# Performance work log

Measured on AMD Instinct MI355X. Metric: run time of the kernel, lower is better.

## Reference

```python
import jax, jax.numpy as jnp
import numpy as np
import math

D_MODEL, N_HEADS, D_HEAD = 768, 12, 64
INIT_RANGE = 0.02
ROPE_BASE = 10000.0


def _rope_cos_sin(seq_len, d_head, dtype=jnp.float32):
    # theta_j = base^(-2j/d), positions m -> angles [T, d/2]
    inv_freq = 1.0 / (ROPE_BASE ** (jnp.arange(0, d_head, 2, dtype=jnp.float32) / d_head))
    ang = jnp.arange(seq_len, dtype=jnp.float32)[:, None] * inv_freq[None, :]
    return jnp.cos(ang).astype(dtype), jnp.sin(ang).astype(dtype)


def _apply_rope(x, cos, sin):
    # x: [b, t, h, d]; rotate consecutive (even, odd) pairs as complex numbers
    xr, xi = x[..., 0::2], x[..., 1::2]
    c = cos[None, :, None, :]
    s = sin[None, :, None, :]
    out_r = xr * c - xi * s
    out_i = xr * s + xi * c
    return jnp.stack([out_r, out_i], axis=-1).reshape(x.shape)


def setup_inputs() -> dict:
    key = jax.random.key(0)
    ks = jax.random.split(key, 5)
    B, T = 2, 2048
    x = jax.random.normal(ks[0], (B, T, D_MODEL), dtype=jnp.float32)
    W_Q = INIT_RANGE * jax.random.normal(ks[1], (N_HEADS, D_MODEL, D_HEAD), dtype=jnp.float32)
    W_K = INIT_RANGE * jax.random.normal(ks[2], (N_HEADS, D_MODEL, D_HEAD), dtype=jnp.float32)
    W_V = INIT_RANGE * jax.random.normal(ks[3], (N_HEADS, D_MODEL, D_HEAD), dtype=jnp.float32)
    W_O = INIT_RANGE * jax.random.normal(ks[4], (N_HEADS, D_HEAD, D_MODEL), dtype=jnp.float32)
    b_Q = jnp.zeros((N_HEADS, D_HEAD), dtype=jnp.float32)
    b_K = jnp.zeros((N_HEADS, D_HEAD), dtype=jnp.float32)
    b_V = jnp.zeros((N_HEADS, D_HEAD), dtype=jnp.float32)
    b_O = jnp.zeros((D_MODEL,), dtype=jnp.float32)
    return {"normalized_resid_pre": x, "W_Q": W_Q, "b_Q": b_Q, "W_K": W_K, "b_K": b_K,
            "W_V": W_V, "b_V": b_V, "W_O": W_O, "b_O": b_O}


def reference(normalized_resid_pre, W_Q, b_Q, W_K, b_K, W_V, b_V, W_O, b_O):
    x = normalized_resid_pre
    B, T, _ = x.shape
    cos, sin = _rope_cos_sin(T, D_HEAD, x.dtype)
    Q = jnp.einsum('btc,hcd->bthd', x, W_Q) + b_Q
    K = jnp.einsum('btc,hcd->bthd', x, W_K) + b_K
    V = jnp.einsum('btc,hcd->bthd', x, W_V) + b_V
    Q = _apply_rope(Q, cos, sin)
    K = _apply_rope(K, cos, sin)
    scores = jnp.einsum('bqhd,bkhd->bhqk', Q, K) / math.sqrt(D_HEAD)
    # Faithful to source: tril zeros upper triangle, then all exact zeros -> -inf
    tril = jnp.tril(jnp.ones((T, T), dtype=bool))
    z = jnp.where(tril[None, None], scores, 0.0)
    z = jnp.where(z == 0.0, -jnp.inf, z)
    probs = jax.nn.softmax(z, axis=-1)
    o = jnp.einsum('bhqk,bkhd->bqhd', probs, V)
    return jnp.einsum('bqhd,hdm->bqm', o, W_O) + b_O
```

## Files before the change

kernel.cpp:

```cpp
#include <hip/hip_runtime.h>

typedef unsigned short u16;
typedef unsigned int u32;
typedef short bf16x8 __attribute__((ext_vector_type(8)));
typedef float f32x4 __attribute__((ext_vector_type(4)));
typedef float f32x16 __attribute__((ext_vector_type(16)));

#define MFMA(a, b, c) __builtin_amdgcn_mfma_f32_16x16x32_bf16(a, b, c, 0, 0, 0)
#define MFMA32(a, b, c) __builtin_amdgcn_mfma_f32_32x32x16_bf16(a, b, c, 0, 0, 0)

__device__ __forceinline__ u16 f2bf(float f) {
  unsigned int u = __float_as_uint(f);
  u = (u + 0x7FFFu + ((u >> 16) & 1u)) >> 16;
  return (u16)u;
}

#define GLOAD16(gp, lp)                                                        \
  __builtin_amdgcn_global_load_lds(                                            \
      (const __attribute__((address_space(1))) void*)(gp),                     \
      (__attribute__((address_space(3))) void*)(lp), 16, 0, 0)

__global__ __launch_bounds__(256) void prep_all(
    const float* __restrict__ x, const float* __restrict__ WQ,
    const float* __restrict__ WK, const float* __restrict__ WV,
    const float* __restrict__ WO, float* __restrict__ cost, float* __restrict__ sint,
    u16* __restrict__ xb, u16* __restrict__ Wt, u16* __restrict__ WoT) {
  __shared__ float tile[32][33];
  const int bid = blockIdx.x, tid = threadIdx.x;

  if (bid < 256) {
    int idx = bid * 256 + tid;
    int t = idx >> 5, i = idx & 31;
    float invf = expf(-(float)i * 0.28782313662425572f);
    float ang = (float)t * invf;
    cost[idx] = cosf(ang);
    sint[idx] = sinf(ang);
  } else if (bid < 3328) {
    int i = ((bid - 256) * 256 + tid) * 4;
    float4 v = *(const float4*)(x + i);
    ushort4 o = make_ushort4(f2bf(v.x), f2bf(v.y), f2bf(v.z), f2bf(v.w));
    *(ushort4*)(xb + i) = o;
  } else if (bid < 5056) {
    const int pbid = bid - 3328;
    const int z = pbid / 48, rem = pbid - z * 48;
    const int y = rem / 24, xk = rem - y * 24;
    const int qkv = z / 12, h = z - qkv * 12;
    const float* W = (qkv == 0 ? WQ : qkv == 1 ? WK : WV) + (size_t)h * 768 * 64;
    const int k0 = xk * 32, d0 = y * 32;
    const int tx = tid & 31, ty = tid >> 5;
#pragma unroll
    for (int it = 0; it < 4; it++)
      tile[ty + it * 8][tx] = W[(size_t)(k0 + ty + it * 8) * 64 + d0 + tx];
    __syncthreads();
    u16* out = Wt + (size_t)(qkv * 768 + h * 64 + d0) * 768 + k0;
#pragma unroll
    for (int it = 0; it < 4; it++)
      out[(size_t)(ty + it * 8) * 768 + tx] = f2bf(tile[tx][ty + it * 8]);
  } else {
    const int wbid = bid - 5056;
    const int a0 = (wbid % 24) * 32, m0 = (wbid / 24) * 32;
    const int tx = tid & 31, ty = tid >> 5;
#pragma unroll
    for (int it = 0; it < 4; it++)
      tile[ty + it * 8][tx] = WO[(size_t)(a0 + ty + it * 8) * 768 + m0 + tx];
    __syncthreads();
#pragma unroll
    for (int it = 0; it < 4; it++)
      WoT[(size_t)(m0 + ty + it * 8) * 768 + a0 + tx] = f2bf(tile[tx][ty + it * 8]);
  }
}

template <int MODE>
__global__ __launch_bounds__(256) void gemm_bt(
    const u16* __restrict__ A, const u16* __restrict__ Bt, int K, int LDA, int LDB,
    const float* __restrict__ bQ, const float* __restrict__ bK, const float* __restrict__ bV,
    const float* __restrict__ cost, const float* __restrict__ sint,
    u16* __restrict__ Qb, u16* __restrict__ Kb, u16* __restrict__ Vt,
    const float* __restrict__ bO, float* __restrict__ Out) {
  __shared__ u16 As[3][64 * 32];
  __shared__ u16 Bs[3][128 * 32];
  const int tid = threadIdx.x;
  const int w = tid >> 6, l = tid & 63;
  const int lr = l >> 4, lc = l & 15;
  const int wr = w >> 1, wc = w & 1;

  const int id = blockIdx.x;
  const int xcd = id & 7, idx = id >> 3;
  const int m0 = (xcd * 8 + (idx & 7)) * 64;
  const int n0 = (idx >> 3) * 128;

  f32x4 acc[2][4];
#pragma unroll
  for (int mi = 0; mi < 2; mi++)
#pragma unroll
    for (int ni = 0; ni < 4; ni++) acc[mi][ni] = (f32x4){0.f, 0.f, 0.f, 0.f};

  const int srow = w * 16 + (l >> 2);
  const int sg = (l & 3) ^ ((l >> 3) & 3);
  const u16* ga = A + (size_t)(m0 + srow) * LDA + sg * 8;
  const u16* gb = Bt + (size_t)(n0 + srow) * LDB + sg * 8;

#define GSTAGE(t, bi)                                                   \
  {                                                                     \
    const int kk = (t) * 32;                                            \
    GLOAD16(ga + kk, &As[bi][w * 512]);                                 \
    GLOAD16(gb + kk, &Bs[bi][w * 512]);                                 \
    GLOAD16(gb + kk + (size_t)64 * LDB, &Bs[bi][2048 + w * 512]);       \
  }

  const int n = K >> 5;
  GSTAGE(0, 0);
  if (n > 1) GSTAGE(1, 1);

  for (int kt = 0; kt < n; kt++) {
    if (kt + 1 < n) asm volatile("s_waitcnt vmcnt(3)" ::: "memory");
    else            asm volatile("s_waitcnt vmcnt(0)" ::: "memory");
    __builtin_amdgcn_s_barrier();
    __builtin_amdgcn_sched_barrier(0);
    if (kt + 2 < n) GSTAGE(kt + 2, (kt + 2) % 3);

    const char* as = (const char*)As[kt % 3];
    const char* bs = (const char*)Bs[kt % 3];
    bf16x8 af[2], bfr[4];
#pragma unroll
    for (int mi = 0; mi < 2; mi++) {
      const int row = wr * 32 + mi * 16 + lc;
      af[mi] = *(const bf16x8*)(as + row * 64 + ((lr ^ ((row >> 1) & 3)) << 4));
    }
#pragma unroll
    for (int ni = 0; ni < 4; ni++) {
      const int row = wc * 64 + ni * 16 + lc;
      bfr[ni] = *(const bf16x8*)(bs + row * 64 + ((lr ^ ((row >> 1) & 3)) << 4));
    }
    __builtin_amdgcn_s_setprio(1);
#pragma unroll
    for (int mi = 0; mi < 2; mi++)
#pragma unroll
      for (int ni = 0; ni < 4; ni++)
        acc[mi][ni] = MFMA(af[mi], bfr[ni], acc[mi][ni]);
    __builtin_amdgcn_s_setprio(0);
  }
#undef GSTAGE

#pragma unroll
  for (int mi = 0; mi < 2; mi++) {
#pragma unroll
    for (int ni = 0; ni < 4; ni++) {
      const int col = n0 + wc * 64 + ni * 16 + lc;
      const int rowb = m0 + wr * 32 + mi * 16 + lr * 4;
      if (MODE == 0) {
        const int qkv = col / 768;
        const int rem = col - qkv * 768;
        const int h = rem >> 6, d = rem & 63, fi = d >> 1;
        const float bb = (qkv == 0 ? bQ : qkv == 1 ? bK : bV)[rem];
#pragma unroll
        for (int r = 0; r < 4; r++) {
          const int grow = rowb + r;
          const int t = grow & 2047;
          float v = acc[mi][ni][r] + bb;
          float pv = __shfl_xor(v, 1);
          if (qkv < 2) {
            const float c = cost[t * 32 + fi], s = sint[t * 32 + fi];
            float o = (d & 1) ? (pv * s + v * c) : (v * c - pv * s);
            if (qkv == 0) o *= 0.125f;
            (qkv == 0 ? Qb : Kb)[(size_t)grow * 768 + rem] = f2bf(o);
          } else {
            const int bidx = grow >> 11;
            Vt[((size_t)(bidx * 12 + h) * 64 + d) * 2048 + t] = f2bf(v);
          }
        }
      } else {
        const float bb = bO[col];
#pragma unroll
        for (int r = 0; r < 4; r++) {
          const int grow = rowb + r;
          Out[(size_t)grow * 768 + col] = acc[mi][ni][r] + bb;
        }
      }
    }
  }
}

__global__ __launch_bounds__(256, 2) void attn_kernel(
    const u16* __restrict__ Qb, const u16* __restrict__ Kb,
    const u16* __restrict__ Vt, u16* __restrict__ Ob) {
  __shared__ char Kls[4][8192];
  __shared__ char Vls[4][8192];
  char* scratch = (char*)Kls;

  const int id = blockIdx.x + 16 * blockIdx.y;
  const int s_ = id >> 3;
  const int bh = (id & 7) + 8 * (s_ % 3);
  const int xq = s_ / 3;
  const int b = bh / 12, h = bh - b * 12;
  const int tid = threadIdx.x, w = tid >> 6, l = tid & 63;
  const int lq = l & 31, hi = l >> 5;
  const int qhalf = w & 1, grp = w >> 1;

  const u16* kbase = Kb + (size_t)(b * 2048) * 768 + h * 64;
  const u16* vbase = Vt + (size_t)(bh * 64) * 2048;

  const int r8 = l >> 3;
  const int scol8 = (l & 7) ^ r8;
  const u16* ksrc = kbase + (size_t)(w * 16 + r8) * 768 + scol8 * 8;
  const u16* vsrc = vbase + (size_t)(w * 16 + r8) * 2048 + scol8 * 8;

#define STAGE(t, bi)                                                        \
  {                                                                         \
    const size_t ko = (size_t)(t) * 64 * 768;                               \
    const int vo = (t) * 64;                                                \
    GLOAD16(ksrc + ko,            &Kls[bi][w * 2048]);                      \
    GLOAD16(ksrc + ko + 8 * 768,  &Kls[bi][w * 2048 + 1024]);               \
    GLOAD16(vsrc + vo,            &Vls[bi][w * 2048]);                      \
    GLOAD16(vsrc + vo + 8 * 2048, &Vls[bi][w * 2048 + 1024]);               \
  }

  const int fswz = (lq & 7) << 4;

#pragma unroll 1
  for (int half = 0; half < 2; half++) {
    const int qblk = half == 0 ? 31 - xq : xq;
    const int n = qblk + 1;
    const int nsup = (n + 1) >> 1;

    bf16x8 qf[4];
    {
      const u16* qp = Qb + ((size_t)(b * 2048 + qblk * 64 + qhalf * 32 + lq)) * 768 +
                      h * 64 + hi * 8;
#pragma unroll
      for (int c = 0; c < 4; c++) qf[c] = *(const bf16x8*)(qp + c * 16);
    }

    float m_run = -INFINITY, l_run = 0.f;
    f32x16 acc2[2];
    acc2[0] = (f32x16)0.0f;
    acc2[1] = (f32x16)0.0f;

    STAGE(0, 0);
    if (n > 1) STAGE(1, 1);

    for (int p = 0; p < nsup; p++) {
      const int t0 = 2 * p;
      asm volatile("s_waitcnt vmcnt(0)" ::: "memory");
      __builtin_amdgcn_s_barrier();
      __builtin_amdgcn_sched_barrier(0);
      if (t0 + 2 < n) STAGE(t0 + 2, (t0 + 2) & 3);
      if (t0 + 3 < n) STAGE(t0 + 3, (t0 + 3) & 3);

      const int tile = t0 + grp;
      if (tile < n) {
        const int cur = tile & 3;

        f32x16 s2[2];
        s2[0] = (f32x16)0.0f;
        s2[1] = (f32x16)0.0f;
        __builtin_amdgcn_s_setprio(1);
#pragma unroll
        for (int c = 0; c < 4; c++) {
          const int cb = (c * 32 + hi * 16) ^ fswz;
          bf16x8 kf0 = *(const bf16x8*)(&Kls[cur][lq * 128] + cb);
          bf16x8 kf1 = *(const bf16x8*)(&Kls[cur][(32 + lq) * 128] + cb);
          s2[0] = MFMA32(kf0, qf[c], s2[0]);
          s2[1] = MFMA32(kf1, qf[c], s2[1]);
        }
        __builtin_amdgcn_s_setprio(0);

        if (tile == qblk) {
          const int qrel = qhalf * 32 + lq;
#pragma unroll
          for (int kt2 = 0; kt2 < 2; kt2++)
#pragma unroll
            for (int r = 0; r < 16; r++) {
              const int ko = kt2 * 32 + (r & 3) + 8 * (r >> 2) + 4 * hi;
              if (ko > qrel) s2[kt2][r] = -INFINITY;
            }
        }

        float pm = s2[0][0];
#pragma unroll
        for (int r = 1; r < 16; r++) pm = fmaxf(pm, s2[0][r]);
#pragma unroll
        for (int r = 0; r < 16; r++) pm = fmaxf(pm, s2[1][r]);
        pm = fmaxf(pm, __shfl_xor(pm, 32));

        const float mn = fmaxf(m_run, pm);
        const float alpha = __expf(m_run - mn);
        m_run = mn;

        float rs = 0.f;
        u32 pk[2][8];
#pragma unroll
        for (int kt2 = 0; kt2 < 2; kt2++)
#pragma unroll
          for (int j = 0; j < 8; j++) {
            float p0 = __expf(s2[kt2][2 * j] - mn);
            float p1 = __expf(s2[kt2][2 * j + 1] - mn);
            rs += p0 + p1;
            asm("v_cvt_pk_bf16_f32 %0, %1, %2" : "=v"(pk[kt2][j]) : "v"(p0), "v"(p1));
          }
        l_run = l_run * alpha + rs;

        union { u32 u[4]; bf16x8 v; } pf[4];
#pragma unroll
        for (int kq = 0; kq < 4; kq++) {
          const int kt2 = kq >> 1, i0 = 4 * (kq & 1);
          u32 a0 = pk[kt2][i0], b0 = pk[kt2][i0 + 2];
          u32 a1 = pk[kt2][i0 + 1], b1 = pk[kt2][i0 + 3];
          asm("v_permlane32_swap_b32 %0, %1" : "+v"(a0), "+v"(b0));
          asm("v_permlane32_swap_b32 %0, %1" : "+v"(a1), "+v"(b1));
          pf[kq].u[0] = a0; pf[kq].u[1] = a1; pf[kq].u[2] = b0; pf[kq].u[3] = b1;
        }

#pragma unroll
        for (int dh = 0; dh < 2; dh++)
#pragma unroll
          for (int r = 0; r < 16; r++) acc2[dh][r] *= alpha;

        __builtin_amdgcn_s_setprio(1);
#pragma unroll
        for (int dh = 0; dh < 2; dh++) {
          const char* vr = &Vls[cur][(dh * 32 + lq) * 128];
#pragma unroll
          for (int kq = 0; kq < 4; kq++) {
            bf16x8 vf = *(const bf16x8*)(vr + ((kq * 32 + hi * 16) ^ fswz));
            acc2[dh] = MFMA32(vf, pf[kq].v, acc2[dh]);
          }
        }
        __builtin_amdgcn_s_setprio(0);
      }
    }

    asm volatile("s_waitcnt lgkmcnt(0)" ::: "memory");
    __builtin_amdgcn_s_barrier();
    if (grp == 1) {
      float* sc = (float*)scratch + ((size_t)(w - 2) * 64 + l) * 34;
#pragma unroll
      for (int dh = 0; dh < 2; dh++)
#pragma unroll
        for (int r = 0; r < 16; r++) sc[dh * 16 + r] = acc2[dh][r];
      sc[32] = m_run;
      sc[33] = l_run;
    }
    asm volatile("s_waitcnt lgkmcnt(0)" ::: "memory");
    __builtin_amdgcn_s_barrier();
    if (grp == 0) {
      const float* sc = (const float*)scratch + ((size_t)w * 64 + l) * 34;
      const float m1 = sc[32], l1 = sc[33];
      const float M = fmaxf(m_run, m1);
      const float a0 = __expf(m_run - M);
      const float a1 = __expf(m1 - M);
      const float lm = l_run * a0 + l1 * a1;
      const float lt = lm + __shfl_xor(lm, 32);
      const float inv = 1.0f / lt;
      u16* ob = Ob + ((size_t)(b * 2048 + qblk * 64 + qhalf * 32 + lq)) * 768 + h * 64;
#pragma unroll
      for (int dh = 0; dh < 2; dh++)
#pragma unroll
        for (int g = 0; g < 4; g++) {
          ushort4 o4;
          o4.x = f2bf((acc2[dh][4 * g + 0] * a0 + sc[dh * 16 + 4 * g + 0] * a1) * inv);
          o4.y = f2bf((acc2[dh][4 * g + 1] * a0 + sc[dh * 16 + 4 * g + 1] * a1) * inv);
          o4.z = f2bf((acc2[dh][4 * g + 2] * a0 + sc[dh * 16 + 4 * g + 2] * a1) * inv);
          o4.w = f2bf((acc2[dh][4 * g + 3] * a0 + sc[dh * 16 + 4 * g + 3] * a1) * inv);
          *(ushort4*)(ob + dh * 32 + 8 * g + 4 * hi) = o4;
        }
    }
    asm volatile("s_waitcnt lgkmcnt(0)" ::: "memory");
    __builtin_amdgcn_s_barrier();
  }
#undef STAGE
}


extern "C" void kernel_launch(void* const* d_in, const int* in_sizes, int n_in,
                              void* d_out, int out_size, void* d_ws, size_t ws_size,
                              hipStream_t stream) {
  const float* x  = (const float*)d_in[0];
  const float* WQ = (const float*)d_in[1];
  const float* bQ = (const float*)d_in[2];
  const float* WK = (const float*)d_in[3];
  const float* bK = (const float*)d_in[4];
  const float* WV = (const float*)d_in[5];
  const float* bV = (const float*)d_in[6];
  const float* WO = (const float*)d_in[7];
  const float* bO = (const float*)d_in[8];

  char* ws = (char*)d_ws;
  u16* Xb    = (u16*)(ws + 0);
  u16* Wqkv  = (u16*)(ws + 6291456);
  u16* WoT   = (u16*)(ws + 9830400);
  u16* Qb    = (u16*)(ws + 11010048);
  u16* Kb    = (u16*)(ws + 17301504);
  u16* Vt    = (u16*)(ws + 23592960);
  u16* Ob    = (u16*)(ws + 29884416);
  float* cost = (float*)(ws + 36175872);
  float* sint = (float*)(ws + 36438016);

  prep_all<<<5632, 256, 0, stream>>>(x, WQ, WK, WV, WO, cost, sint, Xb, Wqkv, WoT);

  gemm_bt<0><<<1152, 256, 0, stream>>>(Xb, Wqkv, 768, 768, 768,
                                       bQ, bK, bV, cost, sint,
                                       Qb, Kb, Vt, nullptr, nullptr);
  attn_kernel<<<dim3(16, 24), 256, 0, stream>>>(Qb, Kb, Vt, Ob);
  gemm_bt<1><<<384, 256, 0, stream>>>(Ob, WoT, 768, 768, 768,
                                      nullptr, nullptr, nullptr, nullptr, nullptr,
                                      nullptr, nullptr, nullptr, bO, (float*)d_out);
}
```

Measured before the change: 107.3 us.

## Enlarge QKV GEMM tile with register-direct A loads; defer softmax rescale

```diff
diff --git a/kernel.cpp b/kernel.cpp
--- a/kernel.cpp
+++ b/kernel.cpp
@@ -70,12 +70,114 @@
   }
 }
 
-template <int MODE>
-__global__ __launch_bounds__(256) void gemm_bt(
-    const u16* __restrict__ A, const u16* __restrict__ Bt, int K, int LDA, int LDB,
+__global__ __launch_bounds__(256) void gemm_qkv(
+    const u16* __restrict__ A, const u16* __restrict__ Bt,
     const float* __restrict__ bQ, const float* __restrict__ bK, const float* __restrict__ bV,
     const float* __restrict__ cost, const float* __restrict__ sint,
-    u16* __restrict__ Qb, u16* __restrict__ Kb, u16* __restrict__ Vt,
+    u16* __restrict__ Qb, u16* __restrict__ Kb, u16* __restrict__ Vt) {
+  __shared__ u16 Bs[3][128 * 32];
+  const int tid = threadIdx.x;
+  const int w = tid >> 6, l = tid & 63;
+  const int lr = l >> 4, lc = l & 15;
+  const int wr = w >> 1, wc = w & 1;
+
+  const int id = blockIdx.x;
+  const int xcd = id & 7, idx = id >> 3;
+  const int m0 = (xcd * 4 + (idx & 3)) * 128;
+  const int n0 = (idx >> 2) * 128;
+
+  f32x4 acc[4][4];
+#pragma unroll
+  for (int mi = 0; mi < 4; mi++)
+#pragma unroll
+    for (int ni = 0; ni < 4; ni++) acc[mi][ni] = (f32x4){0.f, 0.f, 0.f, 0.f};
+
+  const int srow = w * 16 + (l >> 2);
+  const int sg = (l & 3) ^ ((l >> 3) & 3);
+  const u16* gb = Bt + (size_t)(n0 + srow) * 768 + sg * 8;
+  const u16* gA = A + (size_t)(m0 + wr * 64 + lc) * 768 + lr * 8;
+
+#define BSTAGE(t, bi)                                                   \
+  {                                                                     \
+    const int kk = (t) * 32;                                            \
+    GLOAD16(gb + kk, &Bs[bi][w * 512]);                                 \
+    GLOAD16(gb + kk + (size_t)64 * 768, &Bs[bi][2048 + w * 512]);       \
+  }
+#define ALOAD(dst, t)                                                   \
+  {                                                                     \
+    _Pragma("unroll")                                                   \
+    for (int mi = 0; mi < 4; mi++)                                      \
+      dst[mi] = *(const bf16x8*)(gA + (size_t)(mi * 16) * 768 + (t) * 32); \
+  }
+#define KITER(kt, afc, afn)                                                    \
+  {                                                                            \
+    asm volatile("s_waitcnt vmcnt(0)" ::: "memory");                           \
+    __builtin_amdgcn_s_barrier();                                              \
+    __builtin_amdgcn_sched_barrier(0);                                         \
+    if ((kt) + 2 < 24) BSTAGE((kt) + 2, ((kt) + 2) % 3);                       \
+    if ((kt) + 1 < 24) ALOAD(afn, (kt) + 1);                                   \
+    const char* bs = (const char*)Bs[(kt) % 3];                                \
+    bf16x8 bfr[4];                                                             \
+    _Pragma("unroll")                                                          \
+    for (int ni = 0; ni < 4; ni++) {                                           \
+      const int row = wc * 64 + ni * 16 + lc;                                  \
+      bfr[ni] = *(const bf16x8*)(bs + row * 64 + ((lr ^ ((row >> 1) & 3)) << 4)); \
+    }                                                                          \
+    __builtin_amdgcn_s_setprio(1);                                             \
+    _Pragma("unroll")                                                          \
+    for (int mi = 0; mi < 4; mi++)                                             \
+      _Pragma("unroll")                                                        \
+      for (int ni = 0; ni < 4; ni++)                                           \
+        acc[mi][ni] = MFMA(afc[mi], bfr[ni], acc[mi][ni]);                     \
+    __builtin_amdgcn_s_setprio(0);                                             \
+  }
+
+  bf16x8 afA[4], afB[4];
+  BSTAGE(0, 0);
+  BSTAGE(1, 1);
+  ALOAD(afA, 0);
+
+#pragma unroll 1
+  for (int p = 0; p < 12; p++) {
+    KITER(2 * p, afA, afB);
+    KITER(2 * p + 1, afB, afA);
+  }
+#undef KITER
+#undef ALOAD
+#undef BSTAGE
+
+#pragma unroll
+  for (int mi = 0; mi < 4; mi++) {
+#pragma unroll
+    for (int ni = 0; ni < 4; ni++) {
+      const int col = n0 + wc * 64 + ni * 16 + lc;
+      const int rowb = m0 + wr * 64 + mi * 16 + lr * 4;
+      const int qkv = col / 768;
+      const int rem = col - qkv * 768;
+      const int h = rem >> 6, d = rem & 63, fi = d >> 1;
+      const float bb = (qkv == 0 ? bQ : qkv == 1 ? bK : bV)[rem];
+#pragma unroll
+      for (int r = 0; r < 4; r++) {
+        const int grow = rowb + r;
+        const int t = grow & 2047;
+        float v = acc[mi][ni][r] + bb;
+        float pv = __shfl_xor(v, 1);
+        if (qkv < 2) {
+          const float c = cost[t * 32 + fi], s = sint[t * 32 + fi];
+          float o = (d & 1) ? (pv * s + v * c) : (v * c - pv * s);
+          if (qkv == 0) o *= 0.125f;
+          (qkv == 0 ? Qb : Kb)[(size_t)grow * 768 + rem] = f2bf(o);
+        } else {
+          const int bidx = grow >> 11;
+          Vt[((size_t)(bidx * 12 + h) * 64 + d) * 2048 + t] = f2bf(v);
+        }
+      }
+    }
+  }
+}
+
+__global__ __launch_bounds__(256) void gemm_out(
+    const u16* __restrict__ A, const u16* __restrict__ Bt,
     const float* __restrict__ bO, float* __restrict__ Out) {
   __shared__ u16 As[3][64 * 32];
   __shared__ u16 Bs[3][128 * 32];
@@ -97,27 +199,27 @@
 
   const int srow = w * 16 + (l >> 2);
   const int sg = (l & 3) ^ ((l >> 3) & 3);
-  const u16* ga = A + (size_t)(m0 + srow) * LDA + sg * 8;
-  const u16* gb = Bt + (size_t)(n0 + srow) * LDB + sg * 8;
+  const u16* ga = A + (size_t)(m0 + srow) * 768 + sg * 8;
+  const u16* gb = Bt + (size_t)(n0 + srow) * 768 + sg * 8;
 
 #define GSTAGE(t, bi)                                                   \
   {                                                                     \
     const int kk = (t) * 32;                                            \
     GLOAD16(ga + kk, &As[bi][w * 512]);                                 \
     GLOAD16(gb + kk, &Bs[bi][w * 512]);                                 \
-    GLOAD16(gb + kk + (size_t)64 * LDB, &Bs[bi][2048 + w * 512]);       \
-  }
-
-  const int n = K >> 5;
+    GLOAD16(gb + kk + (size_t)64 * 768, &Bs[bi][2048 + w * 512]);       \
+  }
+
+  const int nt = 24;
   GSTAGE(0, 0);
-  if (n > 1) GSTAGE(1, 1);
-
-  for (int kt = 0; kt < n; kt++) {
-    if (kt + 1 < n) asm volatile("s_waitcnt vmcnt(3)" ::: "memory");
-    else            asm volatile("s_waitcnt vmcnt(0)" ::: "memory");
+  GSTAGE(1, 1);
+
+  for (int kt = 0; kt < nt; kt++) {
+    if (kt + 1 < nt) asm volatile("s_waitcnt vmcnt(3)" ::: "memory");
+    else             asm volatile("s_waitcnt vmcnt(0)" ::: "memory");
     __builtin_amdgcn_s_barrier();
     __builtin_amdgcn_sched_barrier(0);
-    if (kt + 2 < n) GSTAGE(kt + 2, (kt + 2) % 3);
+    if (kt + 2 < nt) GSTAGE(kt + 2, (kt + 2) % 3);
 
     const char* as = (const char*)As[kt % 3];
     const char* bs = (const char*)Bs[kt % 3];
@@ -148,34 +250,11 @@
     for (int ni = 0; ni < 4; ni++) {
       const int col = n0 + wc * 64 + ni * 16 + lc;
       const int rowb = m0 + wr * 32 + mi * 16 + lr * 4;
-      if (MODE == 0) {
-        const int qkv = col / 768;
-        const int rem = col - qkv * 768;
-        const int h = rem >> 6, d = rem & 63, fi = d >> 1;
-        const float bb = (qkv == 0 ? bQ : qkv == 1 ? bK : bV)[rem];
-#pragma unroll
-        for (int r = 0; r < 4; r++) {
-          const int grow = rowb + r;
-          const int t = grow & 2047;
-          float v = acc[mi][ni][r] + bb;
-          float pv = __shfl_xor(v, 1);
-          if (qkv < 2) {
-            const float c = cost[t * 32 + fi], s = sint[t * 32 + fi];
-            float o = (d & 1) ? (pv * s + v * c) : (v * c - pv * s);
-            if (qkv == 0) o *= 0.125f;
-            (qkv == 0 ? Qb : Kb)[(size_t)grow * 768 + rem] = f2bf(o);
-          } else {
-            const int bidx = grow >> 11;
-            Vt[((size_t)(bidx * 12 + h) * 64 + d) * 2048 + t] = f2bf(v);
-          }
-        }
-      } else {
-        const float bb = bO[col];
-#pragma unroll
-        for (int r = 0; r < 4; r++) {
-          const int grow = rowb + r;
-          Out[(size_t)grow * 768 + col] = acc[mi][ni][r] + bb;
-        }
+      const float bb = bO[col];
+#pragma unroll
+      for (int r = 0; r < 4; r++) {
+        const int grow = rowb + r;
+        Out[(size_t)grow * 768 + col] = acc[mi][ni][r] + bb;
       }
     }
   }
@@ -283,9 +362,17 @@
         for (int r = 0; r < 16; r++) pm = fmaxf(pm, s2[1][r]);
         pm = fmaxf(pm, __shfl_xor(pm, 32));
 
-        const float mn = fmaxf(m_run, pm);
-        const float alpha = __expf(m_run - mn);
-        m_run = mn;
+        const bool defer = __all(pm <= m_run + 8.0f);
+        if (!defer) {
+          const float mn = fmaxf(m_run, pm);
+          const float alpha = __expf(m_run - mn);
+          m_run = mn;
+          l_run *= alpha;
+#pragma unroll
+          for (int dh = 0; dh < 2; dh++)
+#pragma unroll
+            for (int r = 0; r < 16; r++) acc2[dh][r] *= alpha;
+        }
 
         float rs = 0.f;
         u32 pk[2][8];
@@ -293,12 +380,12 @@
         for (int kt2 = 0; kt2 < 2; kt2++)
 #pragma unroll
           for (int j = 0; j < 8; j++) {
-            float p0 = __expf(s2[kt2][2 * j] - mn);
-            float p1 = __expf(s2[kt2][2 * j + 1] - mn);
+            float p0 = __expf(s2[kt2][2 * j] - m_run);
+            float p1 = __expf(s2[kt2][2 * j + 1] - m_run);
             rs += p0 + p1;
             asm("v_cvt_pk_bf16_f32 %0, %1, %2" : "=v"(pk[kt2][j]) : "v"(p0), "v"(p1));
           }
-        l_run = l_run * alpha + rs;
+        l_run += rs;
 
         union { u32 u[4]; bf16x8 v; } pf[4];
 #pragma unroll
@@ -310,11 +397,6 @@
           asm("v_permlane32_swap_b32 %0, %1" : "+v"(a1), "+v"(b1));
           pf[kq].u[0] = a0; pf[kq].u[1] = a1; pf[kq].u[2] = b0; pf[kq].u[3] = b1;
         }
-
-#pragma unroll
-        for (int dh = 0; dh < 2; dh++)
-#pragma unroll
-          for (int r = 0; r < 16; r++) acc2[dh][r] *= alpha;
 
         __builtin_amdgcn_s_setprio(1);
 #pragma unroll
@@ -398,11 +480,7 @@
 
   prep_all<<<5632, 256, 0, stream>>>(x, WQ, WK, WV, WO, cost, sint, Xb, Wqkv, WoT);
 
-  gemm_bt<0><<<1152, 256, 0, stream>>>(Xb, Wqkv, 768, 768, 768,
-                                       bQ, bK, bV, cost, sint,
-                                       Qb, Kb, Vt, nullptr, nullptr);
+  gemm_qkv<<<576, 256, 0, stream>>>(Xb, Wqkv, bQ, bK, bV, cost, sint, Qb, Kb, Vt);
   attn_kernel<<<dim3(16, 24), 256, 0, stream>>>(Qb, Kb, Vt, Ob);
-  gemm_bt<1><<<384, 256, 0, stream>>>(Ob, WoT, 768, 768, 768,
-                                      nullptr, nullptr, nullptr, nullptr, nullptr,
-                                      nullptr, nullptr, nullptr, bO, (float*)d_out);
-}
+  gemm_out<<<384, 256, 0, stream>>>(Ob, WoT, bO, (float*)d_out);
+}
```

Result: slower. 118.2 us (+10.1%).
